# Kernel optimization log

Hardware: AMD Instinct MI355X
Metric: run time of the kernel (lower is better)

Reference implementation:

```python
import jax, jax.numpy as jnp
import numpy as np

K = 3
PAD = 1


def conv3x3(x, w):
    # x: [B,C,H,W], w: [O,C,3,3] -> [B,O,H,W], stride 1, pad 1, no bias
    return jax.lax.conv_general_dilated(
        x, w, window_strides=(1, 1), padding=((PAD, PAD), (PAD, PAD)),
        dimension_numbers=("NCHW", "OIHW", "NCHW"))


def bilinear_gather(x, py, px):
    """Zero-padded bilinear sampling (torchvision deform_conv2d semantics).
    x: [B,C,H,W]; py, px: [B,KK,H,W] absolute sampling coords.
    Returns [B,C,KK,H,W]."""
    B, C, H, W = x.shape
    KK = py.shape[1]
    y0 = jnp.floor(py)
    x0 = jnp.floor(px)
    wy1 = py - y0  # frac weights
    wx1 = px - x0
    wy0 = 1.0 - wy1
    wx0 = 1.0 - wx1
    x_flat = x.reshape(B, C, H * W)

    def corner(yi, xi, w):
        valid = (yi >= 0) & (yi <= H - 1) & (xi >= 0) & (xi <= W - 1)
        yc = jnp.clip(yi, 0, H - 1).astype(jnp.int32)
        xc = jnp.clip(xi, 0, W - 1).astype(jnp.int32)
        idx = (yc * W + xc).reshape(B, 1, KK * H * W)
        v = jnp.take_along_axis(x_flat, jnp.broadcast_to(idx, (B, C, KK * H * W)), axis=2)
        v = v.reshape(B, C, KK, H, W)
        return v * (w * valid.astype(x.dtype))[:, None]

    return (corner(y0, x0, wy0 * wx0) + corner(y0, x0 + 1.0, wy0 * wx1)
            + corner(y0 + 1.0, x0, wy1 * wx0) + corner(y0 + 1.0, x0 + 1.0, wy1 * wx1))


def deform_conv2d(x, offset, weight):
    """x: [B,C,H,W]; offset: [B,2*K*K,H,W] (dy,dx interleaved per tap, row-major);
    weight: [O,C,K,K]. stride 1, pad 1, dilation 1, 1 group, 1 offset group."""
    B, C, H, W = x.shape
    O = weight.shape[0]
    off = offset.reshape(B, K * K, 2, H, W)
    dy, dx = off[:, :, 0], off[:, :, 1]  # [B,9,H,W]
    ki, kj = jnp.meshgrid(jnp.arange(K, dtype=x.dtype), jnp.arange(K, dtype=x.dtype), indexing="ij")
    ki = ki.reshape(1, K * K, 1, 1)
    kj = kj.reshape(1, K * K, 1, 1)
    hh = jnp.arange(H, dtype=x.dtype).reshape(1, 1, H, 1)
    ww = jnp.arange(W, dtype=x.dtype).reshape(1, 1, 1, W)
    py = hh - PAD + ki + dy  # [B,9,H,W]
    px = ww - PAD + kj + dx
    sampled = bilinear_gather(x, py, px)  # [B,C,9,H,W]
    return jnp.einsum("bckhw,ock->bohw", sampled, weight.reshape(O, C, K * K))


def offset_estimator(x, w1, w2, w3):
    # channel-preserving bottleneck stand-in for Dynamic_offset_estimator
    h = jax.nn.relu(conv3x3(x, w1))
    h = jax.nn.relu(conv3x3(h, w2))
    return conv3x3(h, w3)


def setup_inputs() -> dict:
    key = jax.random.key(0)
    ks = jax.random.split(key, 7)
    B, C, H, W = 1, 768, 64, 64
    C2, CM = 2 * C, 192
    f32 = jnp.float32
    inp = {
        "input_features": jax.random.normal(ks[0], (B, C, H, W), dtype=f32),
        "reference_features": jax.random.normal(ks[1], (B, C, H, W), dtype=f32),
        "est_w1": jax.random.normal(ks[2], (CM, C2, K, K), dtype=f32) / np.sqrt(C2 * K * K),
        "est_w2": jax.random.normal(ks[3], (CM, CM, K, K), dtype=f32) / np.sqrt(CM * K * K),
        "est_w3": jax.random.normal(ks[4], (C2, CM, K, K), dtype=f32) / np.sqrt(CM * K * K),
        "offset_w": jax.random.normal(ks[5], (18, C2, K, K), dtype=f32) / np.sqrt(C2 * K * K),
        "deform_w": jax.random.normal(ks[6], (C, C, K, K), dtype=f32) / np.sqrt(C * K * K),
    }
    return inp


def reference(input_features, reference_features, est_w1, est_w2, est_w3, offset_w, deform_w):
    input_offset = jnp.concatenate([input_features, reference_features], axis=1)  # [B,2C,H,W]
    est = offset_estimator(input_offset, est_w1, est_w2, est_w3)  # [B,2C,H,W]
    offset = conv3x3(est, offset_w)  # [B,18,H,W]
    return deform_conv2d(reference_features, offset, deform_w)  # [B,C,H,W]
```

## Files before the change

### kernel.cpp

```cpp
#include <hip/hip_runtime.h>

#define HWPX 4096

typedef short s8v  __attribute__((ext_vector_type(8)));
typedef float f4v  __attribute__((ext_vector_type(4)));

__device__ inline unsigned short f2bf(float f) {
    unsigned u = __float_as_uint(f);
    return (unsigned short)((u + 0x7fffu + ((u >> 16) & 1u)) >> 16);
}
__device__ inline float bf2f(unsigned s) {
    return __uint_as_float(s << 16);
}

#define GLDS16(gsrc, ldst) \
    __builtin_amdgcn_global_load_lds( \
        (const __attribute__((address_space(1))) unsigned int*)(gsrc), \
        (__attribute__((address_space(3))) unsigned int*)(ldst), 16, 0, 0)

__global__ __launch_bounds__(256)
void tr_cat_k(const float* __restrict__ xa, const float* __restrict__ xb,
              short* __restrict__ xt)
{
    __shared__ __align__(16) short T[64 * 72];
    const int c0 = blockIdx.x * 64, p0 = blockIdx.y * 64, tid = threadIdx.x;
    for (int i = tid; i < 4096; i += 256) {
        int cl = i >> 6, pl = i & 63;
        int c = c0 + cl;
        float v = (c < 768) ? xa[(size_t)c * HWPX + p0 + pl]
                            : xb[(size_t)(c - 768) * HWPX + p0 + pl];
        T[pl * 72 + cl] = (short)f2bf(v);
    }
    __syncthreads();
    for (int i = tid; i < 512; i += 256) {
        int pl = i >> 3, part = i & 7;
        uint4 v = *(const uint4*)&T[pl * 72 + part * 8];
        *(uint4*)&xt[(size_t)(p0 + pl) * 1536 + c0 + part * 8] = v;
    }
}

__device__ inline void wpack1(const float* __restrict__ src, short* __restrict__ dst,
                              int i, int Cin, int Cout, int S, int NB)
{
    int e = i & 7, lane = (i >> 3) & 63;
    int lm = lane & 15, quad = lane >> 4;
    int rest = i >> 9;
    int f = rest % NB;
    int s = (rest / NB) % S;
    int g = rest / (NB * S);
    int cout = g * (NB * 16) + f * 16 + lm;
    int cb = s / 9, t = s % 9;
    int ch = cb * 32 + quad * 8 + e;
    dst[i] = (cout < Cout) ? (short)f2bf(src[((size_t)cout * Cin + ch) * 9 + t]) : 0;
}

#define C1 2654208
#define C2 2985984
#define C3 5640192
#define C4 6082560
#define C5 11390976

__global__ __launch_bounds__(256)
void wpack_all_k(const float* __restrict__ s1, const float* __restrict__ s2,
                 const float* __restrict__ s3, const float* __restrict__ s4,
                 const float* __restrict__ s5,
                 short* __restrict__ d1, short* __restrict__ d2,
                 short* __restrict__ d3, short* __restrict__ d4,
                 short* __restrict__ d5)
{
    int i = blockIdx.x * 256 + threadIdx.x;
    if (i < C1)      wpack1(s1, d1, i,      1536, 192,  432, 4);
    else if (i < C2) wpack1(s2, d2, i - C1, 192,  192,  54,  4);
    else if (i < C3) wpack1(s3, d3, i - C2, 192,  1536, 54,  4);
    else if (i < C4) wpack1(s4, d4, i - C3, 1536, 18,   432, 2);
    else if (i < C5) wpack1(s5, d5, i - C4, 768,  768,  216, 4);
}

template<int NB>
__global__ __launch_bounds__(256, 3)
void convf_k(const short* __restrict__ Xt, int CinStr,
             const short* __restrict__ Wp, int S, int chunks,
             short* __restrict__ Out, int Cstr, int splitStride)
{
    __shared__ __align__(16) short sH[6 * 66 * 40];
    const int tid = threadIdx.x, lane = tid & 63, wv = tid >> 6;
    const int lm = lane & 15, quad = lane >> 4;
    const int r0 = blockIdx.x * 4;
    const int g  = blockIdx.y;
    const int cb0 = blockIdx.z * chunks;
    short* out = Out + (size_t)blockIdx.z * splitStride;

    f4v acc[4][NB];
#pragma unroll
    for (int ma = 0; ma < 4; ++ma)
#pragma unroll
        for (int nb = 0; nb < NB; ++nb)
#pragma unroll
            for (int r = 0; r < 4; ++r) acc[ma][nb][r] = 0.f;

    for (int cc = 0; cc < chunks; ++cc) {
        const int cb = cb0 + cc;
        const short* wpB = Wp + ((size_t)(g * S + cb * 9) * NB) * 512 + lane * 8;
        s8v bb[NB];
#pragma unroll
        for (int f = 0; f < NB; ++f)
            bb[f] = *(const s8v*)&wpB[(size_t)f * 512];

        for (int i = tid; i < 1584; i += 256) {
            int slot = i >> 2, part = i & 3;
            int hr = slot / 66, px = slot % 66;
            int gy = r0 - 1 + hr, gx = px - 1;
            uint4 v = {0, 0, 0, 0};
            if (gy >= 0 && gy < 64 && gx >= 0 && gx < 64)
                v = *(const uint4*)&Xt[(size_t)(gy * 64 + gx) * CinStr + cb * 32 + part * 8];
            *(uint4*)&sH[slot * 40 + part * 8] = v;
        }
        __syncthreads();

#pragma unroll
        for (int t = 0; t < 9; ++t) {
            const int ty = t / 3, tx = t % 3;
            s8v nxt[NB];
#pragma unroll
            for (int f = 0; f < NB; ++f)
                nxt[f] = *(const s8v*)&wpB[(size_t)((t + 1) * NB + f) * 512];
            s8v a[4];
#pragma unroll
            for (int ma = 0; ma < 4; ++ma)
                a[ma] = *(const s8v*)&sH[((wv + ty) * 66 + ma * 16 + lm + tx) * 40 + quad * 8];
#pragma unroll
            for (int ma = 0; ma < 4; ++ma)
#pragma unroll
                for (int nb = 0; nb < NB; ++nb)
                    acc[ma][nb] = __builtin_amdgcn_mfma_f32_16x16x32_bf16(
                        a[ma], bb[nb], acc[ma][nb], 0, 0, 0);
#pragma unroll
            for (int f = 0; f < NB; ++f) bb[f] = nxt[f];
        }
        __syncthreads();
    }

    const int py = (r0 + wv) * 64;
#pragma unroll
    for (int ma = 0; ma < 4; ++ma)
#pragma unroll
        for (int nb = 0; nb < NB; ++nb)
#pragma unroll
            for (int r = 0; r < 4; ++r)
                out[(size_t)(py + ma * 16 + quad * 4 + r) * Cstr
                    + g * (NB * 16) + nb * 16 + lm] = (short)f2bf(acc[ma][nb][r]);
}

__global__ __launch_bounds__(256)
void ep_sumb_k(const short* __restrict__ P, short* __restrict__ outb,
               int nsplit, size_t splitStride, int n8, int relu)
{
    int i = blockIdx.x * 256 + threadIdx.x;
    if (i >= n8) return;
    size_t base = (size_t)i * 8;
    float s[8];
#pragma unroll
    for (int j = 0; j < 8; ++j) s[j] = 0.f;
    for (int sp = 0; sp < nsplit; ++sp) {
        uint4 v = *(const uint4*)&P[sp * splitStride + base];
        s[0] += bf2f(v.x & 0xffffu); s[1] += bf2f(v.x >> 16);
        s[2] += bf2f(v.y & 0xffffu); s[3] += bf2f(v.y >> 16);
        s[4] += bf2f(v.z & 0xffffu); s[5] += bf2f(v.z >> 16);
        s[6] += bf2f(v.w & 0xffffu); s[7] += bf2f(v.w >> 16);
    }
    if (relu) {
#pragma unroll
        for (int j = 0; j < 8; ++j) s[j] = fmaxf(s[j], 0.f);
    }
    uint4 o;
    o.x = f2bf(s[0]) | ((unsigned)f2bf(s[1]) << 16);
    o.y = f2bf(s[2]) | ((unsigned)f2bf(s[3]) << 16);
    o.z = f2bf(s[4]) | ((unsigned)f2bf(s[5]) << 16);
    o.w = f2bf(s[6]) | ((unsigned)f2bf(s[7]) << 16);
    *(uint4*)&outb[base] = o;
}

__global__ __launch_bounds__(256)
void ep_offs_k(const short* __restrict__ P, float* __restrict__ offs, int nsplit)
{
    int i = blockIdx.x * 256 + threadIdx.x;
    if (i >= 18 * HWPX) return;
    int m = i >> 12, px = i & 4095;
    float s = 0.f;
    for (int sp = 0; sp < nsplit; ++sp)
        s += bf2f((unsigned short)P[((size_t)sp * HWPX + px) * 32 + m]);
    offs[i] = s;
}

__global__ __launch_bounds__(256)
void sample_k(const short* __restrict__ xcat, const float* __restrict__ offs,
              short* __restrict__ Smp)
{
    __shared__ int   s_mi[9][16][4];
    __shared__ float s_mw[9][16][4];
    const int tid = threadIdx.x;
    const int p0  = blockIdx.x * 16;
    const int cbq = blockIdx.y * 6;
    const int wv  = tid >> 6, lane = tid & 63;
    const int lmx = lane & 15, qd = lane >> 4;
    const int pg  = p0 >> 6, ma = (p0 >> 4) & 3;

    if (tid < 144) {
        int t = tid / 16, p = tid % 16;
        int pxg = p0 + p;
        int r = pxg >> 6, x = pxg & 63;
        float dy = offs[(size_t)(2 * t)     * HWPX + pxg];
        float dx = offs[(size_t)(2 * t + 1) * HWPX + pxg];
        float py  = (float)(r - 1 + t / 3) + dy;
        float pxf = (float)(x - 1 + t % 3) + dx;
        py  = fminf(fmaxf(py,  -1e6f), 1e6f);
        pxf = fminf(fmaxf(pxf, -1e6f), 1e6f);
        float y0f = floorf(py), x0f = floorf(pxf);
        float wy1 = py - y0f, wx1 = pxf - x0f;
        float wy0 = 1.f - wy1, wx0 = 1.f - wx1;
        bool vy0 = (y0f >=  0.f) && (y0f <= 63.f);
        bool vy1 = (y0f >= -1.f) && (y0f <= 62.f);
        bool vx0 = (x0f >=  0.f) && (x0f <= 63.f);
        bool vx1 = (x0f >= -1.f) && (x0f <= 62.f);
        int y0 = (int)fminf(fmaxf(y0f,       0.f), 63.f);
        int y1 = (int)fminf(fmaxf(y0f + 1.f, 0.f), 63.f);
        int x0 = (int)fminf(fmaxf(x0f,       0.f), 63.f);
        int x1 = (int)fminf(fmaxf(x0f + 1.f, 0.f), 63.f);
        s_mi[t][p][0] = y0 * 64 + x0;  s_mw[t][p][0] = (vy0 && vx0) ? wy0 * wx0 : 0.f;
        s_mi[t][p][1] = y0 * 64 + x1;  s_mw[t][p][1] = (vy0 && vx1) ? wy0 * wx1 : 0.f;
        s_mi[t][p][2] = y1 * 64 + x0;  s_mw[t][p][2] = (vy1 && vx0) ? wy1 * wx0 : 0.f;
        s_mi[t][p][3] = y1 * 64 + x1;  s_mw[t][p][3] = (vy1 && vx1) ? wy1 * wx1 : 0.f;
    }
    __syncthreads();

    for (int j = wv; j < 54; j += 4) {
        const int t = j / 6, cb = cbq + j % 6;
        int   mi[4];
        float mw[4];
#pragma unroll
        for (int c = 0; c < 4; ++c) {
            mi[c] = s_mi[t][lmx][c];
            mw[c] = s_mw[t][lmx][c];
        }
        float a[8];
#pragma unroll
        for (int k = 0; k < 8; ++k) a[k] = 0.f;
#pragma unroll
        for (int c = 0; c < 4; ++c) {
            float wgt = mw[c];
            const short* src = xcat + (size_t)mi[c] * 1536 + 768 + cb * 32 + qd * 8;
            uint4 v = *(const uint4*)src;
            a[0] += wgt * bf2f(v.x & 0xffffu); a[1] += wgt * bf2f(v.x >> 16);
            a[2] += wgt * bf2f(v.y & 0xffffu); a[3] += wgt * bf2f(v.y >> 16);
            a[4] += wgt * bf2f(v.z & 0xffffu); a[5] += wgt * bf2f(v.z >> 16);
            a[6] += wgt * bf2f(v.w & 0xffffu); a[7] += wgt * bf2f(v.w >> 16);
        }
        uint4 o;
        o.x = f2bf(a[0]) | ((unsigned)f2bf(a[1]) << 16);
        o.y = f2bf(a[2]) | ((unsigned)f2bf(a[3]) << 16);
        o.z = f2bf(a[4]) | ((unsigned)f2bf(a[5]) << 16);
        o.w = f2bf(a[6]) | ((unsigned)f2bf(a[7]) << 16);
        size_t addr = ((((size_t)pg * 216 + cb * 9 + t) * 4 + ma) * 64 + lane) * 8;
        *(uint4*)&Smp[addr] = o;
    }
}

__global__ __launch_bounds__(256, 3)
void dgemm_k(const short* __restrict__ Ap, const short* __restrict__ Bp,
             short* __restrict__ P)
{
    __shared__ __align__(16) short sL[3 * 8192];

    const int tid = threadIdx.x, lane = tid & 63, wv = tid >> 6;
    const int lm = lane & 15, quad = lane >> 4;
    const int mg = blockIdx.y * 2 + (wv >> 1);
    const int pg = blockIdx.x * 2 + (wv & 1);
    const int s0 = blockIdx.z * 54;

    const short* stSrc;
    int stChunk;
    if (wv < 2) {
        stSrc = Ap + ((size_t)(blockIdx.y * 2 + wv) * 216 + s0) * 2048;
        stChunk = wv * 2048;
    } else {
        stSrc = Bp + ((size_t)(blockIdx.x * 2 + (wv - 2)) * 216 + s0) * 2048;
        stChunk = 4096 + (wv - 2) * 2048;
    }

    f4v acc[4][4];
#pragma unroll
    for (int ma = 0; ma < 4; ++ma)
#pragma unroll
        for (int nb = 0; nb < 4; ++nb)
#pragma unroll
            for (int r = 0; r < 4; ++r) acc[ma][nb][r] = 0.f;

#pragma unroll
    for (int j = 0; j < 4; ++j)
        GLDS16(stSrc + (size_t)0 * 2048 + j * 512 + lane * 8,
               &sL[0 * 8192 + stChunk + j * 512]);
#pragma unroll
    for (int j = 0; j < 4; ++j)
        GLDS16(stSrc + (size_t)1 * 2048 + j * 512 + lane * 8,
               &sL[1 * 8192 + stChunk + j * 512]);
    asm volatile("s_waitcnt vmcnt(4)" ::: "memory");

    int c0 = 0, c1 = 1, c2 = 2;
    const int aOff = (wv >> 1) * 2048;
    const int bOff = 4096 + (wv & 1) * 2048;

    for (int s = 0; s < 54; ++s) {
        __builtin_amdgcn_s_barrier();
        __builtin_amdgcn_sched_barrier(0);

        s8v av[4], bv[4];
        const int base = c0 * 8192;
#pragma unroll
        for (int f = 0; f < 4; ++f) {
            av[f] = *(const s8v*)&sL[base + aOff + f * 512 + lane * 8];
            bv[f] = *(const s8v*)&sL[base + bOff + f * 512 + lane * 8];
        }

        if (s < 52) {
#pragma unroll
            for (int j = 0; j < 4; ++j)
                GLDS16(stSrc + (size_t)(s + 2) * 2048 + j * 512 + lane * 8,
                       &sL[c2 * 8192 + stChunk + j * 512]);
        }

#pragma unroll
        for (int ma = 0; ma < 4; ++ma)
#pragma unroll
            for (int nb = 0; nb < 4; ++nb)
                acc[ma][nb] = __builtin_amdgcn_mfma_f32_16x16x32_bf16(
                    av[ma], bv[nb], acc[ma][nb], 0, 0, 0);

        if (s < 52) asm volatile("s_waitcnt vmcnt(4)" ::: "memory");
        else        asm volatile("s_waitcnt vmcnt(0)" ::: "memory");

        int t = c0; c0 = c1; c1 = c2; c2 = t;
    }

    short* p = P + (size_t)blockIdx.z * 768 * HWPX;
#pragma unroll
    for (int ma = 0; ma < 4; ++ma)
#pragma unroll
        for (int nb = 0; nb < 4; ++nb)
#pragma unroll
            for (int r = 0; r < 4; ++r)
                p[(size_t)(mg * 64 + ma * 16 + quad * 4 + r) * HWPX
                  + pg * 64 + nb * 16 + lm] = (short)f2bf(acc[ma][nb][r]);
}

__global__ __launch_bounds__(256)
void ep_dg_k(const short* __restrict__ P, float* __restrict__ out)
{
    int i = blockIdx.x * 256 + threadIdx.x;
    if (i >= 768 * HWPX / 8) return;
    size_t base = (size_t)i * 8;
    float s[8];
#pragma unroll
    for (int j = 0; j < 8; ++j) s[j] = 0.f;
    for (int sp = 0; sp < 4; ++sp) {
        uint4 v = *(const uint4*)&P[(size_t)sp * 768 * HWPX + base];
        s[0] += bf2f(v.x & 0xffffu); s[1] += bf2f(v.x >> 16);
        s[2] += bf2f(v.y & 0xffffu); s[3] += bf2f(v.y >> 16);
        s[4] += bf2f(v.z & 0xffffu); s[5] += bf2f(v.z >> 16);
        s[6] += bf2f(v.w & 0xffffu); s[7] += bf2f(v.w >> 16);
    }
    float4 o0 = make_float4(s[0], s[1], s[2], s[3]);
    float4 o1 = make_float4(s[4], s[5], s[6], s[7]);
    *(float4*)&out[base]     = o0;
    *(float4*)&out[base + 4] = o1;
}

extern "C" void kernel_launch(void* const* d_in, const int* in_sizes, int n_in,
                              void* d_out, int out_size, void* d_ws, size_t ws_size,
                              hipStream_t stream)
{
    const float* x_in  = (const float*)d_in[0];
    const float* x_ref = (const float*)d_in[1];
    const float* w1    = (const float*)d_in[2];
    const float* w2    = (const float*)d_in[3];
    const float* w3    = (const float*)d_in[4];
    const float* ow    = (const float*)d_in[5];
    const float* dw    = (const float*)d_in[6];
    float* out = (float*)d_out;

    char* w = (char*)d_ws;
    size_t off = 0;
    auto carve = [&](size_t bytes) {
        void* p = w + off;
        off += (bytes + 255) & ~(size_t)255;
        return p;
    };
    short* xcat = (short*)carve((size_t)4096 * 1536 * 2);
    short* w1p  = (short*)carve((size_t)C1 * 2);
    short* w2p  = (short*)carve((size_t)(C2 - C1) * 2);
    short* w3p  = (short*)carve((size_t)(C3 - C2) * 2);
    short* w4p  = (short*)carve((size_t)(C4 - C3) * 2);
    short* dwp  = (short*)carve((size_t)(C5 - C4) * 2);
    float* offs = (float*)carve((size_t)18 * 4096 * 4);
    short* Smp  = (short*)carve((size_t)4096 * 6912 * 2);
    char*  R    = (char*)carve((size_t)2 * 768 * 4096 * 4);
    short* rh1  = (short*)R;
    short* rh2  = (short*)(R + 1572864);
    short* est  = (short*)(R + 3145728);
    short* Pcv  = Smp;
    short* Pdg  = (short*)R;

    tr_cat_k<<<dim3(24, 64), 256, 0, stream>>>(x_in, x_ref, xcat);
    wpack_all_k<<<(C5 + 255) / 256, 256, 0, stream>>>(w1, w2, w3, ow, dw,
                                                      w1p, w2p, w3p, w4p, dwp);

    const int n8 = 4096 * 192 / 8;
    convf_k<4><<<dim3(16, 3, 16), 256, 0, stream>>>(xcat, 1536, w1p, 432, 3,
                                                    Pcv, 192, 4096 * 192);
    ep_sumb_k<<<(n8 + 255) / 256, 256, 0, stream>>>(Pcv, rh1, 16, (size_t)4096 * 192, n8, 1);
    convf_k<4><<<dim3(16, 3, 6), 256, 0, stream>>>(rh1, 192, w2p, 54, 1,
                                                   Pcv, 192, 4096 * 192);
    ep_sumb_k<<<(n8 + 255) / 256, 256, 0, stream>>>(Pcv, rh2, 6, (size_t)4096 * 192, n8, 1);
    convf_k<4><<<dim3(16, 24, 2), 256, 0, stream>>>(rh2, 192, w3p, 54, 3,
                                                    Pcv, 1536, 4096 * 1536);
    {
        const int n8c3 = 4096 * 1536 / 8;
        ep_sumb_k<<<(n8c3 + 255) / 256, 256, 0, stream>>>(Pcv, est, 2, (size_t)4096 * 1536, n8c3, 0);
    }
    convf_k<2><<<dim3(16, 1, 48), 256, 0, stream>>>(est, 1536, w4p, 432, 1,
                                                    Pcv, 32, 4096 * 32);
    ep_offs_k<<<(18 * HWPX + 255) / 256, 256, 0, stream>>>(Pcv, offs, 48);
    sample_k<<<dim3(256, 4), 256, 0, stream>>>(xcat, offs, Smp);
    dgemm_k<<<dim3(32, 6, 4), 256, 0, stream>>>(dwp, Smp, Pdg);
    ep_dg_k<<<(768 * HWPX / 8 + 255) / 256, 256, 0, stream>>>(Pdg, out);
}
```

Baseline: 334.2 us.

## Widen deform GEMM tile to 128x256 and split K six ways

The deformable-conv GEMM block tile grows from 128x128 to 128x256, giving each wave a 64x128 accumulator, so the LDS ring buffer and per-stage copies grow to match. The split-K factor changes from 4 to 6, with 36 steps per split, and two of the partial-sum slabs go into the now-unused xcat buffer. The epilogue sums six bf16 partials instead of four. The aim is more A-operand reuse and fewer blocks, at the cost of higher register and LDS pressure (occupancy hint lowered to 2) and extra partial-sum traffic in the reduction.

```diff
diff --git a/kernel.cpp b/kernel.cpp
--- a/kernel.cpp
+++ b/kernel.cpp
@@ -265,95 +265,100 @@
     }
 }
 
-__global__ __launch_bounds__(256, 3)
+__global__ __launch_bounds__(256, 2)
 void dgemm_k(const short* __restrict__ Ap, const short* __restrict__ Bp,
-             short* __restrict__ P)
-{
-    __shared__ __align__(16) short sL[3 * 8192];
+             short* __restrict__ P0, short* __restrict__ P1)
+{
+    __shared__ __align__(16) short sL[3 * 12288];
 
     const int tid = threadIdx.x, lane = tid & 63, wv = tid >> 6;
     const int lm = lane & 15, quad = lane >> 4;
     const int mg = blockIdx.y * 2 + (wv >> 1);
-    const int pg = blockIdx.x * 2 + (wv & 1);
-    const int s0 = blockIdx.z * 54;
-
-    const short* stSrc;
-    int stChunk;
-    if (wv < 2) {
-        stSrc = Ap + ((size_t)(blockIdx.y * 2 + wv) * 216 + s0) * 2048;
-        stChunk = wv * 2048;
-    } else {
-        stSrc = Bp + ((size_t)(blockIdx.x * 2 + (wv - 2)) * 216 + s0) * 2048;
-        stChunk = 4096 + (wv - 2) * 2048;
-    }
-
-    f4v acc[4][4];
+    const int pgbase = blockIdx.x * 4 + (wv & 1) * 2;
+    const int s0 = blockIdx.z * 36;
+
+    const short* srcU[6];
+    int dstU[6];
+#pragma unroll
+    for (int u = 0; u < 6; ++u) {
+        int id = wv * 6 + u;
+        int c = id >> 2, j = id & 3;
+        const short* base = (c < 2)
+            ? Ap + ((size_t)(blockIdx.y * 2 + c) * 216 + s0) * 2048
+            : Bp + ((size_t)(blockIdx.x * 4 + (c - 2)) * 216 + s0) * 2048;
+        srcU[u] = base + j * 512 + lane * 8;
+        dstU[u] = ((c < 2) ? c * 2048 : 4096 + (c - 2) * 2048) + j * 512;
+    }
+
+    f4v acc[4][8];
 #pragma unroll
     for (int ma = 0; ma < 4; ++ma)
 #pragma unroll
-        for (int nb = 0; nb < 4; ++nb)
+        for (int nb = 0; nb < 8; ++nb)
 #pragma unroll
             for (int r = 0; r < 4; ++r) acc[ma][nb][r] = 0.f;
 
 #pragma unroll
-    for (int j = 0; j < 4; ++j)
-        GLDS16(stSrc + (size_t)0 * 2048 + j * 512 + lane * 8,
-               &sL[0 * 8192 + stChunk + j * 512]);
-#pragma unroll
-    for (int j = 0; j < 4; ++j)
-        GLDS16(stSrc + (size_t)1 * 2048 + j * 512 + lane * 8,
-               &sL[1 * 8192 + stChunk + j * 512]);
-    asm volatile("s_waitcnt vmcnt(4)" ::: "memory");
+    for (int u = 0; u < 6; ++u)
+        GLDS16(srcU[u], &sL[0 * 12288 + dstU[u]]);
+#pragma unroll
+    for (int u = 0; u < 6; ++u)
+        GLDS16(srcU[u] + 2048, &sL[1 * 12288 + dstU[u]]);
+    asm volatile("s_waitcnt vmcnt(6)" ::: "memory");
 
     int c0 = 0, c1 = 1, c2 = 2;
     const int aOff = (wv >> 1) * 2048;
-    const int bOff = 4096 + (wv & 1) * 2048;
-
-    for (int s = 0; s < 54; ++s) {
+    const int bOff = 4096 + (wv & 1) * 4096;
+
+    for (int s = 0; s < 36; ++s) {
         __builtin_amdgcn_s_barrier();
         __builtin_amdgcn_sched_barrier(0);
 
-        s8v av[4], bv[4];
-        const int base = c0 * 8192;
-#pragma unroll
-        for (int f = 0; f < 4; ++f) {
+        s8v av[4], bv[8];
+        const int base = c0 * 12288;
+#pragma unroll
+        for (int f = 0; f < 4; ++f)
             av[f] = *(const s8v*)&sL[base + aOff + f * 512 + lane * 8];
-            bv[f] = *(const s8v*)&sL[base + bOff + f * 512 + lane * 8];
+#pragma unroll
+        for (int nb = 0; nb < 8; ++nb)
+            bv[nb] = *(const s8v*)&sL[base + bOff + nb * 512 + lane * 8];
+
+        if (s < 34) {
+#pragma unroll
+            for (int u = 0; u < 6; ++u)
+                GLDS16(srcU[u] + (size_t)(s + 2) * 2048, &sL[c2 * 12288 + dstU[u]]);
         }
 
-        if (s < 52) {
-#pragma unroll
-            for (int j = 0; j < 4; ++j)
-                GLDS16(stSrc + (size_t)(s + 2) * 2048 + j * 512 + lane * 8,
-                       &sL[c2 * 8192 + stChunk + j * 512]);
-        }
-
 #pragma unroll
         for (int ma = 0; ma < 4; ++ma)
 #pragma unroll
-            for (int nb = 0; nb < 4; ++nb)
+            for (int nb = 0; nb < 8; ++nb)
                 acc[ma][nb] = __builtin_amdgcn_mfma_f32_16x16x32_bf16(
                     av[ma], bv[nb], acc[ma][nb], 0, 0, 0);
 
-        if (s < 52) asm volatile("s_waitcnt vmcnt(4)" ::: "memory");
+        if (s < 34) asm volatile("s_waitcnt vmcnt(6)" ::: "memory");
         else        asm volatile("s_waitcnt vmcnt(0)" ::: "memory");
 
         int t = c0; c0 = c1; c1 = c2; c2 = t;
     }
 
-    short* p = P + (size_t)blockIdx.z * 768 * HWPX;
+    short* p = (blockIdx.z < 4)
+             ? P0 + (size_t)blockIdx.z * 768 * HWPX
+             : P1 + (size_t)(blockIdx.z - 4) * 768 * HWPX;
 #pragma unroll
     for (int ma = 0; ma < 4; ++ma)
 #pragma unroll
-        for (int nb = 0; nb < 4; ++nb)
+        for (int nb = 0; nb < 8; ++nb)
 #pragma unroll
             for (int r = 0; r < 4; ++r)
                 p[(size_t)(mg * 64 + ma * 16 + quad * 4 + r) * HWPX
-                  + pg * 64 + nb * 16 + lm] = (short)f2bf(acc[ma][nb][r]);
-}
-
-__global__ __launch_bounds__(256)
-void ep_dg_k(const short* __restrict__ P, float* __restrict__ out)
+                  + (pgbase + (nb >> 2)) * 64 + (nb & 3) * 16 + lm]
+                    = (short)f2bf(acc[ma][nb][r]);
+}
+
+__global__ __launch_bounds__(256)
+void ep_dg_k(const short* __restrict__ P0, const short* __restrict__ P1,
+             float* __restrict__ out)
 {
     int i = blockIdx.x * 256 + threadIdx.x;
     if (i >= 768 * HWPX / 8) return;
@@ -361,8 +366,11 @@
     float s[8];
 #pragma unroll
     for (int j = 0; j < 8; ++j) s[j] = 0.f;
-    for (int sp = 0; sp < 4; ++sp) {
-        uint4 v = *(const uint4*)&P[(size_t)sp * 768 * HWPX + base];
+    for (int sp = 0; sp < 6; ++sp) {
+        const short* P = (sp < 4)
+                       ? P0 + (size_t)sp * 768 * HWPX
+                       : P1 + (size_t)(sp - 4) * 768 * HWPX;
+        uint4 v = *(const uint4*)&P[base];
         s[0] += bf2f(v.x & 0xffffu); s[1] += bf2f(v.x >> 16);
         s[2] += bf2f(v.y & 0xffffu); s[3] += bf2f(v.y >> 16);
         s[4] += bf2f(v.z & 0xffffu); s[5] += bf2f(v.z >> 16);
@@ -407,7 +415,8 @@
     short* rh2  = (short*)(R + 1572864);
     short* est  = (short*)(R + 3145728);
     short* Pcv  = Smp;
-    short* Pdg  = (short*)R;
+    short* Pdg0 = (short*)R;
+    short* Pdg1 = xcat;
 
     tr_cat_k<<<dim3(24, 64), 256, 0, stream>>>(x_in, x_ref, xcat);
     wpack_all_k<<<(C5 + 255) / 256, 256, 0, stream>>>(w1, w2, w3, ow, dw,
@@ -430,6 +439,6 @@
                                                     Pcv, 32, 4096 * 32);
     ep_offs_k<<<(18 * HWPX + 255) / 256, 256, 0, stream>>>(Pcv, offs, 48);
     sample_k<<<dim3(256, 4), 256, 0, stream>>>(xcat, offs, Smp);
-    dgemm_k<<<dim3(32, 6, 4), 256, 0, stream>>>(dwp, Smp, Pdg);
-    ep_dg_k<<<(768 * HWPX / 8 + 255) / 256, 256, 0, stream>>>(Pdg, out);
-}
+    dgemm_k<<<dim3(16, 6, 6), 256, 0, stream>>>(dwp, Smp, Pdg0, Pdg1);
+    ep_dg_k<<<(768 * HWPX / 8 + 255) / 256, 256, 0, stream>>>(Pdg0, Pdg1, out);
+}
```

Measured after the change: 333.4 us. No clear change (-0.2%).

## Double-buffer LDS fragment registers in deform GEMM main loop

Applied to the files above, without the earlier changes.

Restructures the GEMM main loop so each thread reads the next stage's A/B fragments from LDS into a second register set while it issues MFMAs on the current set. The loop is unrolled by two over a triple-buffered LDS ring, with the global-to-LDS prefetch issued before the barrier. This is meant to hide LDS read latency behind MFMA work and to remove the per-iteration branch. In exchange it doubles fragment register usage and needs more careful barrier and waitcnt ordering across the three LDS buffers.

```diff
diff --git a/kernel.cpp b/kernel.cpp
--- a/kernel.cpp
+++ b/kernel.cpp
@@ -304,42 +304,93 @@
         GLDS16(stSrc + (size_t)1 * 2048 + j * 512 + lane * 8,
                &sL[1 * 8192 + stChunk + j * 512]);
     asm volatile("s_waitcnt vmcnt(4)" ::: "memory");
-
-    int c0 = 0, c1 = 1, c2 = 2;
+    __builtin_amdgcn_s_barrier();
+    __builtin_amdgcn_sched_barrier(0);
+
     const int aOff = (wv >> 1) * 2048;
     const int bOff = 4096 + (wv & 1) * 2048;
 
-    for (int s = 0; s < 54; ++s) {
+    s8v avA[4], bvA[4], avB[4], bvB[4];
+#pragma unroll
+    for (int f = 0; f < 4; ++f) {
+        avA[f] = *(const s8v*)&sL[0 * 8192 + aOff + f * 512 + lane * 8];
+        bvA[f] = *(const s8v*)&sL[0 * 8192 + bOff + f * 512 + lane * 8];
+    }
+
+    int cA = 0, cB = 1, cC = 2;
+
+    for (int s = 0; s < 52; s += 2) {
+#pragma unroll
+        for (int j = 0; j < 4; ++j)
+            GLDS16(stSrc + (size_t)(s + 2) * 2048 + j * 512 + lane * 8,
+                   &sL[cC * 8192 + stChunk + j * 512]);
+        asm volatile("s_waitcnt vmcnt(4)" ::: "memory");
         __builtin_amdgcn_s_barrier();
         __builtin_amdgcn_sched_barrier(0);
-
-        s8v av[4], bv[4];
-        const int base = c0 * 8192;
-#pragma unroll
-        for (int f = 0; f < 4; ++f) {
-            av[f] = *(const s8v*)&sL[base + aOff + f * 512 + lane * 8];
-            bv[f] = *(const s8v*)&sL[base + bOff + f * 512 + lane * 8];
-        }
-
-        if (s < 52) {
-#pragma unroll
-            for (int j = 0; j < 4; ++j)
-                GLDS16(stSrc + (size_t)(s + 2) * 2048 + j * 512 + lane * 8,
-                       &sL[c2 * 8192 + stChunk + j * 512]);
-        }
-
+        {
+            const int base = cB * 8192;
+#pragma unroll
+            for (int f = 0; f < 4; ++f) {
+                avB[f] = *(const s8v*)&sL[base + aOff + f * 512 + lane * 8];
+                bvB[f] = *(const s8v*)&sL[base + bOff + f * 512 + lane * 8];
+            }
+        }
 #pragma unroll
         for (int ma = 0; ma < 4; ++ma)
 #pragma unroll
             for (int nb = 0; nb < 4; ++nb)
                 acc[ma][nb] = __builtin_amdgcn_mfma_f32_16x16x32_bf16(
-                    av[ma], bv[nb], acc[ma][nb], 0, 0, 0);
-
-        if (s < 52) asm volatile("s_waitcnt vmcnt(4)" ::: "memory");
-        else        asm volatile("s_waitcnt vmcnt(0)" ::: "memory");
-
-        int t = c0; c0 = c1; c1 = c2; c2 = t;
-    }
+                    avA[ma], bvA[nb], acc[ma][nb], 0, 0, 0);
+
+#pragma unroll
+        for (int j = 0; j < 4; ++j)
+            GLDS16(stSrc + (size_t)(s + 3) * 2048 + j * 512 + lane * 8,
+                   &sL[cA * 8192 + stChunk + j * 512]);
+        asm volatile("s_waitcnt vmcnt(4)" ::: "memory");
+        __builtin_amdgcn_s_barrier();
+        __builtin_amdgcn_sched_barrier(0);
+        {
+            const int base = cC * 8192;
+#pragma unroll
+            for (int f = 0; f < 4; ++f) {
+                avA[f] = *(const s8v*)&sL[base + aOff + f * 512 + lane * 8];
+                bvA[f] = *(const s8v*)&sL[base + bOff + f * 512 + lane * 8];
+            }
+        }
+#pragma unroll
+        for (int ma = 0; ma < 4; ++ma)
+#pragma unroll
+            for (int nb = 0; nb < 4; ++nb)
+                acc[ma][nb] = __builtin_amdgcn_mfma_f32_16x16x32_bf16(
+                    avB[ma], bvB[nb], acc[ma][nb], 0, 0, 0);
+
+        int nA = cC, nB = cA, nC = cB;
+        cA = nA; cB = nB; cC = nC;
+    }
+
+    asm volatile("s_waitcnt vmcnt(0)" ::: "memory");
+    __builtin_amdgcn_s_barrier();
+    __builtin_amdgcn_sched_barrier(0);
+    {
+        const int base = cB * 8192;
+#pragma unroll
+        for (int f = 0; f < 4; ++f) {
+            avB[f] = *(const s8v*)&sL[base + aOff + f * 512 + lane * 8];
+            bvB[f] = *(const s8v*)&sL[base + bOff + f * 512 + lane * 8];
+        }
+    }
+#pragma unroll
+    for (int ma = 0; ma < 4; ++ma)
+#pragma unroll
+        for (int nb = 0; nb < 4; ++nb)
+            acc[ma][nb] = __builtin_amdgcn_mfma_f32_16x16x32_bf16(
+                avA[ma], bvA[nb], acc[ma][nb], 0, 0, 0);
+#pragma unroll
+    for (int ma = 0; ma < 4; ++ma)
+#pragma unroll
+        for (int nb = 0; nb < 4; ++nb)
+            acc[ma][nb] = __builtin_amdgcn_mfma_f32_16x16x32_bf16(
+                avB[ma], bvB[nb], acc[ma][nb], 0, 0, 0);
 
     short* p = P + (size_t)blockIdx.z * 768 * HWPX;
 #pragma unroll
```

New measurement: 329.8 us. About the same (-1.3%).
